# Performance work log

Hardware: AMD Instinct MI355X
Metric: run time of the kernel (lower is better)

The kernel has to match this reference:

```python
import jax, jax.numpy as jnp
import numpy as np


def gcn_conv(x, edge_index, W, b):
    # PyG GCNConv: h = x @ W; add self-loops; symmetric D^-1/2 (A+I) D^-1/2 aggregation; + bias
    n = x.shape[0]
    h = x @ W  # [N, out]
    loop = jnp.arange(n, dtype=edge_index.dtype)
    src = jnp.concatenate([edge_index[0], loop])  # message sources
    dst = jnp.concatenate([edge_index[1], loop])  # message targets
    ones = jnp.ones(dst.shape[0], dtype=h.dtype)
    deg = jax.ops.segment_sum(ones, dst, num_segments=n)  # in-degree incl. self-loop
    dinv = jnp.where(deg > 0, jax.lax.rsqrt(deg), 0.0)
    norm = dinv[src] * dinv[dst]  # [E+N]
    msg = h[src] * norm[:, None]  # gather + scale
    out = jax.ops.segment_sum(msg, dst, num_segments=n)  # scatter-add
    return out + b


def setup_inputs() -> dict:
    key = jax.random.key(0)
    ks = jax.random.split(key, 6)
    N, E, D = 100000, 600000, 128
    x = jax.random.normal(ks[0], (N, D), dtype=jnp.float32)
    edge_index = jax.random.randint(ks[1], (2, E), 0, N, dtype=jnp.int64)
    s = 1.0 / np.sqrt(D)
    W1 = jax.random.normal(ks[2], (D, D), dtype=jnp.float32) * s
    b1 = jnp.zeros((D,), dtype=jnp.float32)
    W2 = jax.random.normal(ks[3], (2 * D, D), dtype=jnp.float32) * (1.0 / np.sqrt(2 * D))
    b2 = jnp.zeros((D,), dtype=jnp.float32)
    Wout = jax.random.normal(ks[4], (D, 1), dtype=jnp.float32) * s
    bout = jnp.zeros((1,), dtype=jnp.float32)
    return {"x": x, "edge_index": edge_index, "W1": W1, "b1": b1,
            "W2": W2, "b2": b2, "Wout": Wout, "bout": bout}


def reference(x, edge_index, W1, b1, W2, b2, Wout, bout):
    y = gcn_conv(x, edge_index, W1, b1)          # [N, D]
    y = jnp.concatenate([x, y], axis=-1)          # [N, 2D]
    y = jax.nn.leaky_relu(y, negative_slope=0.01)
    z = gcn_conv(y, edge_index, W2, b2)           # [N, D]
    z = jax.nn.leaky_relu(z, negative_slope=0.01)
    return z @ Wout + bout                        # [N, 1]
```

## Files before the change

kernel.cpp:

```cpp
#include <hip/hip_runtime.h>

#define DIM 128
#define CAP 48

typedef _Float16 half8 __attribute__((ext_vector_type(8)));
typedef float f32x4 __attribute__((ext_vector_type(4)));

__device__ __forceinline__ float lrelu(float v) { return v > 0.f ? v : 0.01f * v; }

__device__ __forceinline__ void gather_sum(
    const _Float16* __restrict__ H, const int* __restrict__ sl,
    int cnt, int g, int zr, float a[8]) {
    int c16 = cnt < 16 ? cnt : 16;
    int sidb = (g < c16) ? sl[g] : zr;
    half8 v[8];
#pragma unroll
    for (int j = 0; j < 8; ++j) {
        int s = __shfl(sidb, j, 16);
        v[j] = *(const half8*)&H[(size_t)s * DIM + g * 8];
    }
#pragma unroll
    for (int j = 0; j < 8; ++j)
#pragma unroll
        for (int e = 0; e < 8; ++e) a[e] += (float)v[j][e];
    if (cnt > 8) {
#pragma unroll
        for (int j = 0; j < 8; ++j) {
            int s = __shfl(sidb, 8 + j, 16);
            v[j] = *(const half8*)&H[(size_t)s * DIM + g * 8];
        }
#pragma unroll
        for (int j = 0; j < 8; ++j)
#pragma unroll
            for (int e = 0; e < 8; ++e) a[e] += (float)v[j][e];
        if (cnt > 16) {
            for (int base = 16; base < cnt; base += 16) {
                int m = cnt - base;
                if (m > 16) m = 16;
                int sb = (g < m) ? sl[base + g] : zr;
                for (int j = 0; j < m; ++j) {
                    int s = __shfl(sb, j, 16);
                    half8 vv = *(const half8*)&H[(size_t)s * DIM + g * 8];
#pragma unroll
                    for (int e = 0; e < 8; ++e) a[e] += (float)vv[e];
                }
            }
        }
    }
}

__global__ __launch_bounds__(256) void k_prep(
    const int* __restrict__ src, const int* __restrict__ dst,
    int* __restrict__ cursor, int* __restrict__ srcs, int e, int eb,
    const float* __restrict__ W1, _Float16* __restrict__ Wp1,
    const float* __restrict__ W2, _Float16* __restrict__ Wp2,
    _Float16* __restrict__ zrow) {
    int b = blockIdx.x;
    if (b < eb) {
        int i = b * 256 + threadIdx.x;
        if (i < e) {
            int d = dst[i];
            int p = atomicAdd(&cursor[d], 1);
            if (p < CAP) srcs[(size_t)d * CAP + p] = src[i];
        }
        return;
    }
    b -= eb;
    if (b >= 192) {
        if (threadIdx.x < 16) {
            half8 z = 0;
            *(half8*)&zrow[threadIdx.x * 8] = z;
        }
        return;
    }
    const float* W;
    _Float16* Wp;
    int tid2;
    if (b < 64) { W = W1; Wp = Wp1; tid2 = b * 256 + threadIdx.x; }
    else        { W = W2; Wp = Wp2; tid2 = (b - 64) * 256 + threadIdx.x; }
    int jj = tid2 & 7;
    int frag = tid2 >> 3;
    int l = frag & 63;
    int cb = (frag >> 6) & 7;
    int kb = frag >> 9;
    int k = kb * 32 + ((l >> 4) << 3) + jj;
    int nn = cb * 16 + (l & 15);
    Wp[tid2] = (_Float16)W[(size_t)k * DIM + nn];
}

__global__ __launch_bounds__(256, 2) void k_mm1(
    const float* __restrict__ x, const _Float16* __restrict__ Wp1,
    const _Float16* __restrict__ Wp2, const int* __restrict__ cursor,
    _Float16* __restrict__ hs, _Float16* __restrict__ P, int n) {
    __shared__ _Float16 Hs[64 * 136];
    const int tid = threadIdx.x;
    const int w = tid >> 6, l = tid & 63;
    const int row0 = blockIdx.x * 64;
    const int arow = row0 + w * 16 + (l & 15);
    const int kq = (l >> 4) << 3;
    const bool ok = arow < n;
    const float* xr = &x[(size_t)arow * DIM + kq];

    f32x4 ah[8], ap[8];
#pragma unroll
    for (int cb = 0; cb < 8; ++cb) {
        f32x4 z = {0.f, 0.f, 0.f, 0.f};
        ah[cb] = z; ap[cb] = z;
    }

#pragma unroll
    for (int kb = 0; kb < 4; ++kb) {
        float4 v0 = make_float4(0.f, 0.f, 0.f, 0.f), v1 = v0;
        if (ok) {
            v0 = *(const float4*)&xr[kb * 32];
            v1 = *(const float4*)&xr[kb * 32 + 4];
        }
        half8 a, al;
        a[0] = (_Float16)v0.x; a[1] = (_Float16)v0.y;
        a[2] = (_Float16)v0.z; a[3] = (_Float16)v0.w;
        a[4] = (_Float16)v1.x; a[5] = (_Float16)v1.y;
        a[6] = (_Float16)v1.z; a[7] = (_Float16)v1.w;
#pragma unroll
        for (int e = 0; e < 8; ++e) {
            _Float16 t = a[e];
            al[e] = (t > (_Float16)0.f) ? t : t * (_Float16)0.01f;
        }
#pragma unroll
        for (int cb = 0; cb < 8; ++cb) {
            half8 bf = *(const half8*)&Wp1[((kb * 8 + cb) * 64 + l) * 8];
            ah[cb] = __builtin_amdgcn_mfma_f32_16x16x32_f16(a, bf, ah[cb], 0, 0, 0);
        }
#pragma unroll
        for (int cb = 0; cb < 8; ++cb) {
            half8 bf = *(const half8*)&Wp2[((kb * 8 + cb) * 64 + l) * 8];
            ap[cb] = __builtin_amdgcn_mfma_f32_16x16x32_f16(al, bf, ap[cb], 0, 0, 0);
        }
    }
    const int orow = w * 16 + ((l >> 4) << 2);
    const int oc = l & 15;
#pragma unroll
    for (int reg = 0; reg < 4; ++reg) {
        int grow = row0 + orow + reg;
        float d = (grow < n) ? rsqrtf((float)cursor[grow] + 1.0f) : 0.f;
#pragma unroll
        for (int cb = 0; cb < 8; ++cb)
            Hs[(orow + reg) * 136 + cb * 16 + oc] = (_Float16)(ah[cb][reg] * d);
    }
    __syncthreads();
#pragma unroll
    for (int it = 0; it < 4; ++it) {
        int i = it * 256 + tid;
        int r = i >> 4, c = (i & 15) * 8;
        if (row0 + r < n)
            *(half8*)&hs[(size_t)(row0 + r) * DIM + c] = *(const half8*)&Hs[r * 136 + c];
    }
    _Float16* pl = P + ((size_t)(blockIdx.x * 4 + w) * 64 + l) * 32;
#pragma unroll
    for (int c = 0; c < 4; ++c) {
        half8 o;
#pragma unroll
        for (int e = 0; e < 4; ++e) {
            o[e]     = (_Float16)ap[2 * c][e];
            o[4 + e] = (_Float16)ap[2 * c + 1][e];
        }
        *(half8*)&pl[c * 8] = o;
    }
}

__global__ __launch_bounds__(256, 2) void k_mm2g(
    const _Float16* __restrict__ hs, const int* __restrict__ cursor,
    const int* __restrict__ srcs, const float* __restrict__ b1,
    const _Float16* __restrict__ Wp2, const _Float16* __restrict__ P,
    _Float16* __restrict__ hs2, int n) {
    __shared__ _Float16 LS[64 * 136];
    const int tid = threadIdx.x;
    const int w = tid >> 6, l = tid & 63;
    const int g = tid & 15, gid = tid >> 4;
    const int row0 = blockIdx.x * 64;

    f32x4 acc[8];
    const _Float16* pl = P + ((size_t)(blockIdx.x * 4 + w) * 64 + l) * 32;
#pragma unroll
    for (int c = 0; c < 4; ++c) {
        half8 pv = *(const half8*)&pl[c * 8];
#pragma unroll
        for (int e = 0; e < 4; ++e) {
            acc[2 * c][e]     = (float)pv[e];
            acc[2 * c + 1][e] = (float)pv[4 + e];
        }
    }

#pragma unroll
    for (int it = 0; it < 4; ++it) {
        int node = row0 + it * 16 + gid;
        half8 o = 0;
        if (node < n) {
            int rawc = cursor[node];
            int cnt = rawc > CAP ? CAP : rawc;
            const int* sl = &srcs[(size_t)node * CAP];
            half8 h = *(const half8*)&hs[(size_t)node * DIM + g * 8];
            float a[8];
#pragma unroll
            for (int e = 0; e < 8; ++e) a[e] = (float)h[e];
            gather_sum(hs, sl, cnt, g, n, a);
            float d = rsqrtf((float)rawc + 1.0f);
            const float4 bb0 = *(const float4*)&b1[g * 8];
            const float4 bb1 = *(const float4*)&b1[g * 8 + 4];
            o[0] = (_Float16)lrelu(fmaf(a[0], d, bb0.x));
            o[1] = (_Float16)lrelu(fmaf(a[1], d, bb0.y));
            o[2] = (_Float16)lrelu(fmaf(a[2], d, bb0.z));
            o[3] = (_Float16)lrelu(fmaf(a[3], d, bb0.w));
            o[4] = (_Float16)lrelu(fmaf(a[4], d, bb1.x));
            o[5] = (_Float16)lrelu(fmaf(a[5], d, bb1.y));
            o[6] = (_Float16)lrelu(fmaf(a[6], d, bb1.z));
            o[7] = (_Float16)lrelu(fmaf(a[7], d, bb1.w));
        }
        *(half8*)&LS[(((it * 4 + (g >> 2)) * 64) + (g & 3) * 16 + gid) * 8] = o;
    }
    __syncthreads();

#pragma unroll
    for (int kb = 0; kb < 4; ++kb) {
        half8 a = *(const half8*)&LS[((w * 4 + kb) * 64 + l) * 8];
#pragma unroll
        for (int cb = 0; cb < 8; ++cb) {
            half8 bf = *(const half8*)&Wp2[(((kb + 4) * 8 + cb) * 64 + l) * 8];
            acc[cb] = __builtin_amdgcn_mfma_f32_16x16x32_f16(a, bf, acc[cb], 0, 0, 0);
        }
    }
    __syncthreads();
    const int orow = w * 16 + ((l >> 4) << 2);
    const int oc = l & 15;
#pragma unroll
    for (int reg = 0; reg < 4; ++reg) {
        int grow = row0 + orow + reg;
        float d = (grow < n) ? rsqrtf((float)cursor[grow] + 1.0f) : 0.f;
#pragma unroll
        for (int cb = 0; cb < 8; ++cb)
            LS[(orow + reg) * 136 + cb * 16 + oc] = (_Float16)(acc[cb][reg] * d);
    }
    __syncthreads();
#pragma unroll
    for (int it = 0; it < 4; ++it) {
        int i = it * 256 + tid;
        int r = i >> 4, c = (i & 15) * 8;
        if (row0 + r < n)
            *(half8*)&hs2[(size_t)(row0 + r) * DIM + c] = *(const half8*)&LS[r * 136 + c];
    }
}

__global__ __launch_bounds__(256) void k_gather2(
    const _Float16* __restrict__ hs2, const int* __restrict__ cursor,
    const int* __restrict__ srcs, const float* __restrict__ b2,
    const float* __restrict__ wout, const float* __restrict__ bout,
    float* __restrict__ out, int n) {
    const int node = blockIdx.x * 16 + (threadIdx.x >> 4);
    const int g = threadIdx.x & 15;
    if (node >= n) return;
    int rawc = cursor[node];
    int cnt = rawc > CAP ? CAP : rawc;
    const int* sl = &srcs[(size_t)node * CAP];
    half8 h = *(const half8*)&hs2[(size_t)node * DIM + g * 8];
    float a[8];
#pragma unroll
    for (int e = 0; e < 8; ++e) a[e] = (float)h[e];
    gather_sum(hs2, sl, cnt, g, n, a);
    float d = rsqrtf((float)rawc + 1.0f);
    const float4 bb0 = *(const float4*)&b2[g * 8];
    const float4 bb1 = *(const float4*)&b2[g * 8 + 4];
    const float4 wv0 = *(const float4*)&wout[g * 8];
    const float4 wv1 = *(const float4*)&wout[g * 8 + 4];
    float s = lrelu(fmaf(a[0], d, bb0.x)) * wv0.x + lrelu(fmaf(a[1], d, bb0.y)) * wv0.y +
              lrelu(fmaf(a[2], d, bb0.z)) * wv0.z + lrelu(fmaf(a[3], d, bb0.w)) * wv0.w +
              lrelu(fmaf(a[4], d, bb1.x)) * wv1.x + lrelu(fmaf(a[5], d, bb1.y)) * wv1.y +
              lrelu(fmaf(a[6], d, bb1.z)) * wv1.z + lrelu(fmaf(a[7], d, bb1.w)) * wv1.w;
#pragma unroll
    for (int off = 8; off > 0; off >>= 1) s += __shfl_down(s, off, 16);
    if (g == 0) out[node] = s + bout[0];
}

extern "C" void kernel_launch(void* const* d_in, const int* in_sizes, int n_in,
                              void* d_out, int out_size, void* d_ws, size_t ws_size,
                              hipStream_t stream) {
    const float* x    = (const float*)d_in[0];
    const int*   ei   = (const int*)d_in[1];
    const float* W1   = (const float*)d_in[2];
    const float* b1   = (const float*)d_in[3];
    const float* W2   = (const float*)d_in[4];
    const float* b2   = (const float*)d_in[5];
    const float* Wout = (const float*)d_in[6];
    const float* bout = (const float*)d_in[7];
    float* out = (float*)d_out;

    const int N = in_sizes[0] / DIM;
    const int E = in_sizes[1] / 2;
    const int* src = ei;
    const int* dst = ei + E;

    const int gb = (N + 63) / 64;
    const long long nx = (long long)N * DIM;

    size_t Na = ((size_t)N + 63) & ~(size_t)63;
    int* cursor   = (int*)d_ws;
    int* srcs     = cursor + Na;
    _Float16* Wp1 = (_Float16*)(srcs + (size_t)N * CAP);
    _Float16* Wp2 = Wp1 + 128 * 128;
    _Float16* hsb = Wp2 + 256 * 128;
    _Float16* Pb  = hsb + nx + DIM;

    const int eb = (E + 255) / 256;

    hipMemsetAsync(cursor, 0, (size_t)N * sizeof(int), stream);
    k_prep<<<eb + 193, 256, 0, stream>>>(src, dst, cursor, srcs, E, eb, W1, Wp1, W2, Wp2,
                                         hsb + nx);
    k_mm1<<<gb, 256, 0, stream>>>(x, Wp1, Wp2, cursor, hsb, Pb, N);
    k_mm2g<<<gb, 256, 0, stream>>>(hsb, cursor, srcs, b1, Wp2, Pb, Pb, N);
    k_gather2<<<(N + 15) / 16, 256, 0, stream>>>(Pb, cursor, srcs, b2, Wout, bout, out, N);
}
```

Before: 228.1 us.

## Fuse all stages into one persistent cooperative kernel with grid syncs

Replaces the memset plus four kernel launches with a single cooperative persistent kernel. It zeroes the cursors, packs the weights, builds the adjacency, runs both matmul/gather stages and the final gather, with grid-wide syncs between phases. The aim is to remove launch overhead and the tail gaps between kernels. In exchange, occupancy is capped by the cooperative grid size (launch_bounds 256,4). Grid syncs add latency, and blocks now loop over tiles, which may reduce latency hiding in the gather phases.

```diff
diff --git a/kernel.cpp b/kernel.cpp
--- a/kernel.cpp
+++ b/kernel.cpp
@@ -1,4 +1,7 @@
 #include <hip/hip_runtime.h>
+#include <hip/hip_cooperative_groups.h>
+
+namespace cg = cooperative_groups;
 
 #define DIM 128
 #define CAP 48
@@ -46,6 +49,245 @@
                 }
             }
         }
+    }
+}
+
+
+__device__ __forceinline__ void mm1_tile(
+    int tb, const float* __restrict__ x, const _Float16* __restrict__ Wp1,
+    const _Float16* __restrict__ Wp2, const int* __restrict__ cursor,
+    _Float16* __restrict__ hs, _Float16* __restrict__ P, int n, _Float16* Hs) {
+    const int tid = threadIdx.x;
+    const int w = tid >> 6, l = tid & 63;
+    const int row0 = tb * 64;
+    const int arow = row0 + w * 16 + (l & 15);
+    const int kq = (l >> 4) << 3;
+    const bool ok = arow < n;
+    const float* xr = &x[(size_t)arow * DIM + kq];
+
+    f32x4 ah[8], ap[8];
+#pragma unroll
+    for (int cb = 0; cb < 8; ++cb) {
+        f32x4 z = {0.f, 0.f, 0.f, 0.f};
+        ah[cb] = z; ap[cb] = z;
+    }
+
+#pragma unroll
+    for (int kb = 0; kb < 4; ++kb) {
+        float4 v0 = make_float4(0.f, 0.f, 0.f, 0.f), v1 = v0;
+        if (ok) {
+            v0 = *(const float4*)&xr[kb * 32];
+            v1 = *(const float4*)&xr[kb * 32 + 4];
+        }
+        half8 a, al;
+        a[0] = (_Float16)v0.x; a[1] = (_Float16)v0.y;
+        a[2] = (_Float16)v0.z; a[3] = (_Float16)v0.w;
+        a[4] = (_Float16)v1.x; a[5] = (_Float16)v1.y;
+        a[6] = (_Float16)v1.z; a[7] = (_Float16)v1.w;
+#pragma unroll
+        for (int e = 0; e < 8; ++e) {
+            _Float16 t = a[e];
+            al[e] = (t > (_Float16)0.f) ? t : t * (_Float16)0.01f;
+        }
+#pragma unroll
+        for (int cb = 0; cb < 8; ++cb) {
+            half8 bf = *(const half8*)&Wp1[((kb * 8 + cb) * 64 + l) * 8];
+            ah[cb] = __builtin_amdgcn_mfma_f32_16x16x32_f16(a, bf, ah[cb], 0, 0, 0);
+        }
+#pragma unroll
+        for (int cb = 0; cb < 8; ++cb) {
+            half8 bf = *(const half8*)&Wp2[((kb * 8 + cb) * 64 + l) * 8];
+            ap[cb] = __builtin_amdgcn_mfma_f32_16x16x32_f16(al, bf, ap[cb], 0, 0, 0);
+        }
+    }
+    const int orow = w * 16 + ((l >> 4) << 2);
+    const int oc = l & 15;
+#pragma unroll
+    for (int reg = 0; reg < 4; ++reg) {
+        int grow = row0 + orow + reg;
+        float d = (grow < n) ? rsqrtf((float)cursor[grow] + 1.0f) : 0.f;
+#pragma unroll
+        for (int cb = 0; cb < 8; ++cb)
+            Hs[(orow + reg) * 136 + cb * 16 + oc] = (_Float16)(ah[cb][reg] * d);
+    }
+    __syncthreads();
+#pragma unroll
+    for (int it = 0; it < 4; ++it) {
+        int i = it * 256 + tid;
+        int r = i >> 4, c = (i & 15) * 8;
+        if (row0 + r < n)
+            *(half8*)&hs[(size_t)(row0 + r) * DIM + c] = *(const half8*)&Hs[r * 136 + c];
+    }
+    _Float16* pl = P + ((size_t)(tb * 4 + w) * 64 + l) * 32;
+#pragma unroll
+    for (int c = 0; c < 4; ++c) {
+        half8 o;
+#pragma unroll
+        for (int e = 0; e < 4; ++e) {
+            o[e]     = (_Float16)ap[2 * c][e];
+            o[4 + e] = (_Float16)ap[2 * c + 1][e];
+        }
+        *(half8*)&pl[c * 8] = o;
+    }
+}
+
+__device__ __forceinline__ void mm2g_tile(
+    int tb, const _Float16* __restrict__ hs, const int* __restrict__ cursor,
+    const int* __restrict__ srcs, const float* __restrict__ b1,
+    const _Float16* __restrict__ Wp2, const _Float16* __restrict__ P,
+    _Float16* __restrict__ hs2, int n, _Float16* LS) {
+    const int tid = threadIdx.x;
+    const int w = tid >> 6, l = tid & 63;
+    const int g = tid & 15, gid = tid >> 4;
+    const int row0 = tb * 64;
+
+    f32x4 acc[8];
+    const _Float16* pl = P + ((size_t)(tb * 4 + w) * 64 + l) * 32;
+#pragma unroll
+    for (int c = 0; c < 4; ++c) {
+        half8 pv = *(const half8*)&pl[c * 8];
+#pragma unroll
+        for (int e = 0; e < 4; ++e) {
+            acc[2 * c][e]     = (float)pv[e];
+            acc[2 * c + 1][e] = (float)pv[4 + e];
+        }
+    }
+
+#pragma unroll
+    for (int it = 0; it < 4; ++it) {
+        int node = row0 + it * 16 + gid;
+        half8 o = 0;
+        if (node < n) {
+            int rawc = cursor[node];
+            int cnt = rawc > CAP ? CAP : rawc;
+            const int* sl = &srcs[(size_t)node * CAP];
+            half8 h = *(const half8*)&hs[(size_t)node * DIM + g * 8];
+            float a[8];
+#pragma unroll
+            for (int e = 0; e < 8; ++e) a[e] = (float)h[e];
+            gather_sum(hs, sl, cnt, g, n, a);
+            float d = rsqrtf((float)rawc + 1.0f);
+            const float4 bb0 = *(const float4*)&b1[g * 8];
+            const float4 bb1 = *(const float4*)&b1[g * 8 + 4];
+            o[0] = (_Float16)lrelu(fmaf(a[0], d, bb0.x));
+            o[1] = (_Float16)lrelu(fmaf(a[1], d, bb0.y));
+            o[2] = (_Float16)lrelu(fmaf(a[2], d, bb0.z));
+            o[3] = (_Float16)lrelu(fmaf(a[3], d, bb0.w));
+            o[4] = (_Float16)lrelu(fmaf(a[4], d, bb1.x));
+            o[5] = (_Float16)lrelu(fmaf(a[5], d, bb1.y));
+            o[6] = (_Float16)lrelu(fmaf(a[6], d, bb1.z));
+            o[7] = (_Float16)lrelu(fmaf(a[7], d, bb1.w));
+        }
+        *(half8*)&LS[(((it * 4 + (g >> 2)) * 64) + (g & 3) * 16 + gid) * 8] = o;
+    }
+    __syncthreads();
+
+#pragma unroll
+    for (int kb = 0; kb < 4; ++kb) {
+        half8 a = *(const half8*)&LS[((w * 4 + kb) * 64 + l) * 8];
+#pragma unroll
+        for (int cb = 0; cb < 8; ++cb) {
+            half8 bf = *(const half8*)&Wp2[(((kb + 4) * 8 + cb) * 64 + l) * 8];
+            acc[cb] = __builtin_amdgcn_mfma_f32_16x16x32_f16(a, bf, acc[cb], 0, 0, 0);
+        }
+    }
+    __syncthreads();
+    const int orow = w * 16 + ((l >> 4) << 2);
+    const int oc = l & 15;
+#pragma unroll
+    for (int reg = 0; reg < 4; ++reg) {
+        int grow = row0 + orow + reg;
+        float d = (grow < n) ? rsqrtf((float)cursor[grow] + 1.0f) : 0.f;
+#pragma unroll
+        for (int cb = 0; cb < 8; ++cb)
+            LS[(orow + reg) * 136 + cb * 16 + oc] = (_Float16)(acc[cb][reg] * d);
+    }
+    __syncthreads();
+#pragma unroll
+    for (int it = 0; it < 4; ++it) {
+        int i = it * 256 + tid;
+        int r = i >> 4, c = (i & 15) * 8;
+        if (row0 + r < n)
+            *(half8*)&hs2[(size_t)(row0 + r) * DIM + c] = *(const half8*)&LS[r * 136 + c];
+    }
+}
+
+__device__ __forceinline__ void gather2_grp(
+    int base, const _Float16* __restrict__ hs2, const int* __restrict__ cursor,
+    const int* __restrict__ srcs, const float* __restrict__ b2,
+    const float* __restrict__ wout, const float* __restrict__ bout,
+    float* __restrict__ out, int n) {
+    const int node = base + (threadIdx.x >> 4);
+    const int g = threadIdx.x & 15;
+    if (node >= n) return;
+    int rawc = cursor[node];
+    int cnt = rawc > CAP ? CAP : rawc;
+    const int* sl = &srcs[(size_t)node * CAP];
+    half8 h = *(const half8*)&hs2[(size_t)node * DIM + g * 8];
+    float a[8];
+#pragma unroll
+    for (int e = 0; e < 8; ++e) a[e] = (float)h[e];
+    gather_sum(hs2, sl, cnt, g, n, a);
+    float d = rsqrtf((float)rawc + 1.0f);
+    const float4 bb0 = *(const float4*)&b2[g * 8];
+    const float4 bb1 = *(const float4*)&b2[g * 8 + 4];
+    const float4 wv0 = *(const float4*)&wout[g * 8];
+    const float4 wv1 = *(const float4*)&wout[g * 8 + 4];
+    float s = lrelu(fmaf(a[0], d, bb0.x)) * wv0.x + lrelu(fmaf(a[1], d, bb0.y)) * wv0.y +
+              lrelu(fmaf(a[2], d, bb0.z)) * wv0.z + lrelu(fmaf(a[3], d, bb0.w)) * wv0.w +
+              lrelu(fmaf(a[4], d, bb1.x)) * wv1.x + lrelu(fmaf(a[5], d, bb1.y)) * wv1.y +
+              lrelu(fmaf(a[6], d, bb1.z)) * wv1.z + lrelu(fmaf(a[7], d, bb1.w)) * wv1.w;
+#pragma unroll
+    for (int off = 8; off > 0; off >>= 1) s += __shfl_down(s, off, 16);
+    if (g == 0) out[node] = s + bout[0];
+}
+
+__global__ __launch_bounds__(256, 4) void k_fused(
+    const float* __restrict__ x, const int* __restrict__ esrc, const int* __restrict__ edst,
+    int E, const float* __restrict__ W1, const float* __restrict__ b1,
+    const float* __restrict__ W2, const float* __restrict__ b2,
+    const float* __restrict__ Wout, const float* __restrict__ bout,
+    float* __restrict__ out, int* __restrict__ cursor, int* __restrict__ srcs,
+    _Float16* __restrict__ Wp1, _Float16* __restrict__ Wp2,
+    _Float16* __restrict__ hs, _Float16* __restrict__ P, int n, int gb) {
+    __shared__ _Float16 LS[64 * 136];
+    const int tid = threadIdx.x;
+    const int nb = gridDim.x;
+    const int gtid = blockIdx.x * 256 + tid;
+    const int gstride = nb * 256;
+
+    for (int i = gtid; i < n; i += gstride) cursor[i] = 0;
+    if (blockIdx.x == 0 && tid < 16) {
+        half8 z = 0;
+        *(half8*)&hs[(size_t)n * DIM + tid * 8] = z;
+    }
+    for (int t = gtid; t < 49152; t += gstride) {
+        const float* W; _Float16* Wp; int t2;
+        if (t < 16384) { W = W1; Wp = Wp1; t2 = t; }
+        else           { W = W2; Wp = Wp2; t2 = t - 16384; }
+        int jj = t2 & 7, frag = t2 >> 3;
+        int l = frag & 63, cb = (frag >> 6) & 7, kb = frag >> 9;
+        Wp[t2] = (_Float16)W[(size_t)(kb * 32 + ((l >> 4) << 3) + jj) * DIM + cb * 16 + (l & 15)];
+    }
+    cg::this_grid().sync();
+    for (int i = gtid; i < E; i += gstride) {
+        int d = edst[i];
+        int p = atomicAdd(&cursor[d], 1);
+        if (p < CAP) srcs[(size_t)d * CAP + p] = esrc[i];
+    }
+    cg::this_grid().sync();
+    for (int tb = blockIdx.x; tb < gb; tb += nb) {
+        mm1_tile(tb, x, Wp1, Wp2, cursor, hs, P, n, LS);
+        __syncthreads();
+    }
+    cg::this_grid().sync();
+    for (int tb = blockIdx.x; tb < gb; tb += nb) {
+        mm2g_tile(tb, hs, cursor, srcs, b1, Wp2, P, P, n, LS);
+        __syncthreads();
+    }
+    cg::this_grid().sync();
+    for (int base = blockIdx.x * 16; base < n; base += nb * 16) {
+        gather2_grp(base, P, cursor, srcs, b2, Wout, bout, out, n);
     }
 }
 
@@ -83,9 +325,7 @@
     int l = frag & 63;
     int cb = (frag >> 6) & 7;
     int kb = frag >> 9;
-    int k = kb * 32 + ((l >> 4) << 3) + jj;
-    int nn = cb * 16 + (l & 15);
-    Wp[tid2] = (_Float16)W[(size_t)k * DIM + nn];
+    Wp[tid2] = (_Float16)W[(size_t)(kb * 32 + ((l >> 4) << 3) + jj) * DIM + cb * 16 + (l & 15)];
 }
 
 __global__ __launch_bounds__(256, 2) void k_mm1(
@@ -93,78 +333,7 @@
     const _Float16* __restrict__ Wp2, const int* __restrict__ cursor,
     _Float16* __restrict__ hs, _Float16* __restrict__ P, int n) {
     __shared__ _Float16 Hs[64 * 136];
-    const int tid = threadIdx.x;
-    const int w = tid >> 6, l = tid & 63;
-    const int row0 = blockIdx.x * 64;
-    const int arow = row0 + w * 16 + (l & 15);
-    const int kq = (l >> 4) << 3;
-    const bool ok = arow < n;
-    const float* xr = &x[(size_t)arow * DIM + kq];
-
-    f32x4 ah[8], ap[8];
-#pragma unroll
-    for (int cb = 0; cb < 8; ++cb) {
-        f32x4 z = {0.f, 0.f, 0.f, 0.f};
-        ah[cb] = z; ap[cb] = z;
-    }
-
-#pragma unroll
-    for (int kb = 0; kb < 4; ++kb) {
-        float4 v0 = make_float4(0.f, 0.f, 0.f, 0.f), v1 = v0;
-        if (ok) {
-            v0 = *(const float4*)&xr[kb * 32];
-            v1 = *(const float4*)&xr[kb * 32 + 4];
-        }
-        half8 a, al;
-        a[0] = (_Float16)v0.x; a[1] = (_Float16)v0.y;
-        a[2] = (_Float16)v0.z; a[3] = (_Float16)v0.w;
-        a[4] = (_Float16)v1.x; a[5] = (_Float16)v1.y;
-        a[6] = (_Float16)v1.z; a[7] = (_Float16)v1.w;
-#pragma unroll
-        for (int e = 0; e < 8; ++e) {
-            _Float16 t = a[e];
-            al[e] = (t > (_Float16)0.f) ? t : t * (_Float16)0.01f;
-        }
-#pragma unroll
-        for (int cb = 0; cb < 8; ++cb) {
-            half8 bf = *(const half8*)&Wp1[((kb * 8 + cb) * 64 + l) * 8];
-            ah[cb] = __builtin_amdgcn_mfma_f32_16x16x32_f16(a, bf, ah[cb], 0, 0, 0);
-        }
-#pragma unroll
-        for (int cb = 0; cb < 8; ++cb) {
-            half8 bf = *(const half8*)&Wp2[((kb * 8 + cb) * 64 + l) * 8];
-            ap[cb] = __builtin_amdgcn_mfma_f32_16x16x32_f16(al, bf, ap[cb], 0, 0, 0);
-        }
-    }
-    const int orow = w * 16 + ((l >> 4) << 2);
-    const int oc = l & 15;
-#pragma unroll
-    for (int reg = 0; reg < 4; ++reg) {
-        int grow = row0 + orow + reg;
-        float d = (grow < n) ? rsqrtf((float)cursor[grow] + 1.0f) : 0.f;
-#pragma unroll
-        for (int cb = 0; cb < 8; ++cb)
-            Hs[(orow + reg) * 136 + cb * 16 + oc] = (_Float16)(ah[cb][reg] * d);
-    }
-    __syncthreads();
-#pragma unroll
-    for (int it = 0; it < 4; ++it) {
-        int i = it * 256 + tid;
-        int r = i >> 4, c = (i & 15) * 8;
-        if (row0 + r < n)
-            *(half8*)&hs[(size_t)(row0 + r) * DIM + c] = *(const half8*)&Hs[r * 136 + c];
-    }
-    _Float16* pl = P + ((size_t)(blockIdx.x * 4 + w) * 64 + l) * 32;
-#pragma unroll
-    for (int c = 0; c < 4; ++c) {
-        half8 o;
-#pragma unroll
-        for (int e = 0; e < 4; ++e) {
-            o[e]     = (_Float16)ap[2 * c][e];
-            o[4 + e] = (_Float16)ap[2 * c + 1][e];
-        }
-        *(half8*)&pl[c * 8] = o;
-    }
+    mm1_tile(blockIdx.x, x, Wp1, Wp2, cursor, hs, P, n, Hs);
 }
 
 __global__ __launch_bounds__(256, 2) void k_mm2g(
@@ -173,80 +342,7 @@
     const _Float16* __restrict__ Wp2, const _Float16* __restrict__ P,
     _Float16* __restrict__ hs2, int n) {
     __shared__ _Float16 LS[64 * 136];
-    const int tid = threadIdx.x;
-    const int w = tid >> 6, l = tid & 63;
-    const int g = tid & 15, gid = tid >> 4;
-    const int row0 = blockIdx.x * 64;
-
-    f32x4 acc[8];
-    const _Float16* pl = P + ((size_t)(blockIdx.x * 4 + w) * 64 + l) * 32;
-#pragma unroll
-    for (int c = 0; c < 4; ++c) {
-        half8 pv = *(const half8*)&pl[c * 8];
-#pragma unroll
-        for (int e = 0; e < 4; ++e) {
-            acc[2 * c][e]     = (float)pv[e];
-            acc[2 * c + 1][e] = (float)pv[4 + e];
-        }
-    }
-
-#pragma unroll
-    for (int it = 0; it < 4; ++it) {
-        int node = row0 + it * 16 + gid;
-        half8 o = 0;
-        if (node < n) {
-            int rawc = cursor[node];
-            int cnt = rawc > CAP ? CAP : rawc;
-            const int* sl = &srcs[(size_t)node * CAP];
-            half8 h = *(const half8*)&hs[(size_t)node * DIM + g * 8];
-            float a[8];
-#pragma unroll
-            for (int e = 0; e < 8; ++e) a[e] = (float)h[e];
-            gather_sum(hs, sl, cnt, g, n, a);
-            float d = rsqrtf((float)rawc + 1.0f);
-            const float4 bb0 = *(const float4*)&b1[g * 8];
-            const float4 bb1 = *(const float4*)&b1[g * 8 + 4];
-            o[0] = (_Float16)lrelu(fmaf(a[0], d, bb0.x));
-            o[1] = (_Float16)lrelu(fmaf(a[1], d, bb0.y));
-            o[2] = (_Float16)lrelu(fmaf(a[2], d, bb0.z));
-            o[3] = (_Float16)lrelu(fmaf(a[3], d, bb0.w));
-            o[4] = (_Float16)lrelu(fmaf(a[4], d, bb1.x));
-            o[5] = (_Float16)lrelu(fmaf(a[5], d, bb1.y));
-            o[6] = (_Float16)lrelu(fmaf(a[6], d, bb1.z));
-            o[7] = (_Float16)lrelu(fmaf(a[7], d, bb1.w));
-        }
-        *(half8*)&LS[(((it * 4 + (g >> 2)) * 64) + (g & 3) * 16 + gid) * 8] = o;
-    }
-    __syncthreads();
-
-#pragma unroll
-    for (int kb = 0; kb < 4; ++kb) {
-        half8 a = *(const half8*)&LS[((w * 4 + kb) * 64 + l) * 8];
-#pragma unroll
-        for (int cb = 0; cb < 8; ++cb) {
-            half8 bf = *(const half8*)&Wp2[(((kb + 4) * 8 + cb) * 64 + l) * 8];
-            acc[cb] = __builtin_amdgcn_mfma_f32_16x16x32_f16(a, bf, acc[cb], 0, 0, 0);
-        }
-    }
-    __syncthreads();
-    const int orow = w * 16 + ((l >> 4) << 2);
-    const int oc = l & 15;
-#pragma unroll
-    for (int reg = 0; reg < 4; ++reg) {
-        int grow = row0 + orow + reg;
-        float d = (grow < n) ? rsqrtf((float)cursor[grow] + 1.0f) : 0.f;
-#pragma unroll
-        for (int cb = 0; cb < 8; ++cb)
-            LS[(orow + reg) * 136 + cb * 16 + oc] = (_Float16)(acc[cb][reg] * d);
-    }
-    __syncthreads();
-#pragma unroll
-    for (int it = 0; it < 4; ++it) {
-        int i = it * 256 + tid;
-        int r = i >> 4, c = (i & 15) * 8;
-        if (row0 + r < n)
-            *(half8*)&hs2[(size_t)(row0 + r) * DIM + c] = *(const half8*)&LS[r * 136 + c];
-    }
+    mm2g_tile(blockIdx.x, hs, cursor, srcs, b1, Wp2, P, hs2, n, LS);
 }
 
 __global__ __launch_bounds__(256) void k_gather2(
@@ -254,29 +350,7 @@
     const int* __restrict__ srcs, const float* __restrict__ b2,
     const float* __restrict__ wout, const float* __restrict__ bout,
     float* __restrict__ out, int n) {
-    const int node = blockIdx.x * 16 + (threadIdx.x >> 4);
-    const int g = threadIdx.x & 15;
-    if (node >= n) return;
-    int rawc = cursor[node];
-    int cnt = rawc > CAP ? CAP : rawc;
-    const int* sl = &srcs[(size_t)node * CAP];
-    half8 h = *(const half8*)&hs2[(size_t)node * DIM + g * 8];
-    float a[8];
-#pragma unroll
-    for (int e = 0; e < 8; ++e) a[e] = (float)h[e];
-    gather_sum(hs2, sl, cnt, g, n, a);
-    float d = rsqrtf((float)rawc + 1.0f);
-    const float4 bb0 = *(const float4*)&b2[g * 8];
-    const float4 bb1 = *(const float4*)&b2[g * 8 + 4];
-    const float4 wv0 = *(const float4*)&wout[g * 8];
-    const float4 wv1 = *(const float4*)&wout[g * 8 + 4];
-    float s = lrelu(fmaf(a[0], d, bb0.x)) * wv0.x + lrelu(fmaf(a[1], d, bb0.y)) * wv0.y +
-              lrelu(fmaf(a[2], d, bb0.z)) * wv0.z + lrelu(fmaf(a[3], d, bb0.w)) * wv0.w +
-              lrelu(fmaf(a[4], d, bb1.x)) * wv1.x + lrelu(fmaf(a[5], d, bb1.y)) * wv1.y +
-              lrelu(fmaf(a[6], d, bb1.z)) * wv1.z + lrelu(fmaf(a[7], d, bb1.w)) * wv1.w;
-#pragma unroll
-    for (int off = 8; off > 0; off >>= 1) s += __shfl_down(s, off, 16);
-    if (g == 0) out[node] = s + bout[0];
+    gather2_grp(blockIdx.x * 16, hs2, cursor, srcs, b2, wout, bout, out, n);
 }
 
 extern "C" void kernel_launch(void* const* d_in, const int* in_sizes, int n_in,
@@ -308,12 +382,41 @@
     _Float16* hsb = Wp2 + 256 * 128;
     _Float16* Pb  = hsb + nx + DIM;
 
-    const int eb = (E + 255) / 256;
-
-    hipMemsetAsync(cursor, 0, (size_t)N * sizeof(int), stream);
-    k_prep<<<eb + 193, 256, 0, stream>>>(src, dst, cursor, srcs, E, eb, W1, Wp1, W2, Wp2,
-                                         hsb + nx);
-    k_mm1<<<gb, 256, 0, stream>>>(x, Wp1, Wp2, cursor, hsb, Pb, N);
-    k_mm2g<<<gb, 256, 0, stream>>>(hsb, cursor, srcs, b1, Wp2, Pb, Pb, N);
-    k_gather2<<<(N + 15) / 16, 256, 0, stream>>>(Pb, cursor, srcs, b2, Wout, bout, out, N);
-}
+    static int coop_blocks = -2;
+    if (coop_blocks == -2) {
+        int nbpc = 0;
+        if (hipOccupancyMaxActiveBlocksPerMultiprocessor(
+                &nbpc, reinterpret_cast<const void*>(k_fused), 256, 0) != hipSuccess || nbpc < 1)
+            nbpc = 0;
+        if (nbpc > 8) nbpc = 8;
+        int ncu = 256;
+        hipDeviceProp_t prop;
+        if (hipGetDeviceProperties(&prop, 0) == hipSuccess && prop.multiProcessorCount > 0)
+            ncu = prop.multiProcessorCount;
+        coop_blocks = nbpc > 0 ? nbpc * ncu : -1;
+    }
+
+    bool launched = false;
+    if (coop_blocks > 0) {
+        int E_ = E, N_ = N, gb_ = gb;
+        void* args[] = {(void*)&x, (void*)&src, (void*)&dst, (void*)&E_,
+                        (void*)&W1, (void*)&b1, (void*)&W2, (void*)&b2,
+                        (void*)&Wout, (void*)&bout, (void*)&out,
+                        (void*)&cursor, (void*)&srcs, (void*)&Wp1, (void*)&Wp2,
+                        (void*)&hsb, (void*)&Pb, (void*)&N_, (void*)&gb_};
+        if (hipLaunchCooperativeKernel(reinterpret_cast<const void*>(k_fused),
+                                       dim3(coop_blocks), dim3(256), args, 0, stream) == hipSuccess)
+            launched = true;
+        else
+            coop_blocks = -1;
+    }
+    if (!launched) {
+        const int eb = (E + 255) / 256;
+        hipMemsetAsync(cursor, 0, (size_t)N * sizeof(int), stream);
+        k_prep<<<eb + 193, 256, 0, stream>>>(src, dst, cursor, srcs, E, eb, W1, Wp1, W2, Wp2,
+                                             hsb + nx);
+        k_mm1<<<gb, 256, 0, stream>>>(x, Wp1, Wp2, cursor, hsb, Pb, N);
+        k_mm2g<<<gb, 256, 0, stream>>>(hsb, cursor, srcs, b1, Wp2, Pb, Pb, N);
+        k_gather2<<<(N + 15) / 16, 256, 0, stream>>>(Pb, cursor, srcs, b2, Wout, bout, out, N);
+    }
+}
```

Measured after the change: 646.1 us. 183% more time.

## Overlap edge bucketing with first matmul and move source normalization into gather

Applied to the files above, without the earlier changes.

Edge bucketing (the atomic cursor increments and srcs writes) moves out of the prep kernel and into extra blocks of the first matmul kernel, so CSR building runs alongside the GEMM. Because degrees are not final during that GEMM, the per-row D^-1/2 scaling of h is dropped there and applied per source inside the layer-1 gather, using a shuffled rsqrt of each neighbor's cursor. The hipMemset is replaced by zeroing inside the init kernel, which removes one stream operation. The cost is an extra cursor load and rsqrt per gathered group, plus an FMA instead of an add per element.

```diff
diff --git a/kernel.cpp b/kernel.cpp
--- a/kernel.cpp
+++ b/kernel.cpp
@@ -49,23 +49,66 @@
     }
 }
 
-__global__ __launch_bounds__(256) void k_prep(
-    const int* __restrict__ src, const int* __restrict__ dst,
-    int* __restrict__ cursor, int* __restrict__ srcs, int e, int eb,
+__device__ __forceinline__ void gather_sum_scaled(
+    const _Float16* __restrict__ H, const int* __restrict__ cursor,
+    const int* __restrict__ sl, int cnt, int g, int zr, float a[8]) {
+    int c16 = cnt < 16 ? cnt : 16;
+    int sidb = (g < c16) ? sl[g] : zr;
+    float dvb = rsqrtf((float)cursor[sidb] + 1.0f);
+    half8 v[8];
+#pragma unroll
+    for (int j = 0; j < 8; ++j) {
+        int s = __shfl(sidb, j, 16);
+        v[j] = *(const half8*)&H[(size_t)s * DIM + g * 8];
+    }
+#pragma unroll
+    for (int j = 0; j < 8; ++j) {
+        float sc = __shfl(dvb, j, 16);
+#pragma unroll
+        for (int e = 0; e < 8; ++e) a[e] = fmaf((float)v[j][e], sc, a[e]);
+    }
+    if (cnt > 8) {
+#pragma unroll
+        for (int j = 0; j < 8; ++j) {
+            int s = __shfl(sidb, 8 + j, 16);
+            v[j] = *(const half8*)&H[(size_t)s * DIM + g * 8];
+        }
+#pragma unroll
+        for (int j = 0; j < 8; ++j) {
+            float sc = __shfl(dvb, 8 + j, 16);
+#pragma unroll
+            for (int e = 0; e < 8; ++e) a[e] = fmaf((float)v[j][e], sc, a[e]);
+        }
+        if (cnt > 16) {
+            for (int base = 16; base < cnt; base += 16) {
+                int m = cnt - base;
+                if (m > 16) m = 16;
+                int sb = (g < m) ? sl[base + g] : zr;
+                float db2 = rsqrtf((float)cursor[sb] + 1.0f);
+                for (int j = 0; j < m; ++j) {
+                    int s = __shfl(sb, j, 16);
+                    float sc = __shfl(db2, j, 16);
+                    half8 vv = *(const half8*)&H[(size_t)s * DIM + g * 8];
+#pragma unroll
+                    for (int e = 0; e < 8; ++e) a[e] = fmaf((float)vv[e], sc, a[e]);
+                }
+            }
+        }
+    }
+}
+
+__global__ __launch_bounds__(256) void k_init(
+    int* __restrict__ cursor, int na, int nzb,
     const float* __restrict__ W1, _Float16* __restrict__ Wp1,
     const float* __restrict__ W2, _Float16* __restrict__ Wp2,
     _Float16* __restrict__ zrow) {
     int b = blockIdx.x;
-    if (b < eb) {
+    if (b < nzb) {
         int i = b * 256 + threadIdx.x;
-        if (i < e) {
-            int d = dst[i];
-            int p = atomicAdd(&cursor[d], 1);
-            if (p < CAP) srcs[(size_t)d * CAP + p] = src[i];
-        }
+        if (i < na) cursor[i] = 0;
         return;
     }
-    b -= eb;
+    b -= nzb;
     if (b >= 192) {
         if (threadIdx.x < 16) {
             half8 z = 0;
@@ -83,19 +126,29 @@
     int l = frag & 63;
     int cb = (frag >> 6) & 7;
     int kb = frag >> 9;
-    int k = kb * 32 + ((l >> 4) << 3) + jj;
-    int nn = cb * 16 + (l & 15);
-    Wp[tid2] = (_Float16)W[(size_t)k * DIM + nn];
-}
-
-__global__ __launch_bounds__(256, 2) void k_mm1(
+    Wp[tid2] = (_Float16)W[(size_t)(kb * 32 + ((l >> 4) << 3) + jj) * DIM + cb * 16 + (l & 15)];
+}
+
+__global__ __launch_bounds__(256, 2) void k_front(
     const float* __restrict__ x, const _Float16* __restrict__ Wp1,
-    const _Float16* __restrict__ Wp2, const int* __restrict__ cursor,
-    _Float16* __restrict__ hs, _Float16* __restrict__ P, int n) {
+    const _Float16* __restrict__ Wp2, _Float16* __restrict__ hs,
+    _Float16* __restrict__ P, int n, int gb,
+    const int* __restrict__ esrc, const int* __restrict__ edst,
+    int* __restrict__ cursor, int* __restrict__ srcs, int E) {
     __shared__ _Float16 Hs[64 * 136];
+    const int bb = blockIdx.x;
+    if (bb >= gb) {
+        int i = (bb - gb) * 256 + threadIdx.x;
+        if (i < E) {
+            int d = edst[i];
+            int p = atomicAdd(&cursor[d], 1);
+            if (p < CAP) srcs[(size_t)d * CAP + p] = esrc[i];
+        }
+        return;
+    }
     const int tid = threadIdx.x;
     const int w = tid >> 6, l = tid & 63;
-    const int row0 = blockIdx.x * 64;
+    const int row0 = bb * 64;
     const int arow = row0 + w * 16 + (l & 15);
     const int kq = (l >> 4) << 3;
     const bool ok = arow < n;
@@ -140,11 +193,9 @@
     const int oc = l & 15;
 #pragma unroll
     for (int reg = 0; reg < 4; ++reg) {
-        int grow = row0 + orow + reg;
-        float d = (grow < n) ? rsqrtf((float)cursor[grow] + 1.0f) : 0.f;
 #pragma unroll
         for (int cb = 0; cb < 8; ++cb)
-            Hs[(orow + reg) * 136 + cb * 16 + oc] = (_Float16)(ah[cb][reg] * d);
+            Hs[(orow + reg) * 136 + cb * 16 + oc] = (_Float16)ah[cb][reg];
     }
     __syncthreads();
 #pragma unroll
@@ -154,7 +205,7 @@
         if (row0 + r < n)
             *(half8*)&hs[(size_t)(row0 + r) * DIM + c] = *(const half8*)&Hs[r * 136 + c];
     }
-    _Float16* pl = P + ((size_t)(blockIdx.x * 4 + w) * 64 + l) * 32;
+    _Float16* pl = P + ((size_t)(bb * 4 + w) * 64 + l) * 32;
 #pragma unroll
     for (int c = 0; c < 4; ++c) {
         half8 o;
@@ -198,12 +249,12 @@
             int rawc = cursor[node];
             int cnt = rawc > CAP ? CAP : rawc;
             const int* sl = &srcs[(size_t)node * CAP];
+            float d = rsqrtf((float)rawc + 1.0f);
             half8 h = *(const half8*)&hs[(size_t)node * DIM + g * 8];
             float a[8];
 #pragma unroll
-            for (int e = 0; e < 8; ++e) a[e] = (float)h[e];
-            gather_sum(hs, sl, cnt, g, n, a);
-            float d = rsqrtf((float)rawc + 1.0f);
+            for (int e = 0; e < 8; ++e) a[e] = (float)h[e] * d;
+            gather_sum_scaled(hs, cursor, sl, cnt, g, n, a);
             const float4 bb0 = *(const float4*)&b1[g * 8];
             const float4 bb1 = *(const float4*)&b1[g * 8 + 4];
             o[0] = (_Float16)lrelu(fmaf(a[0], d, bb0.x));
@@ -309,11 +360,10 @@
     _Float16* Pb  = hsb + nx + DIM;
 
     const int eb = (E + 255) / 256;
-
-    hipMemsetAsync(cursor, 0, (size_t)N * sizeof(int), stream);
-    k_prep<<<eb + 193, 256, 0, stream>>>(src, dst, cursor, srcs, E, eb, W1, Wp1, W2, Wp2,
-                                         hsb + nx);
-    k_mm1<<<gb, 256, 0, stream>>>(x, Wp1, Wp2, cursor, hsb, Pb, N);
+    const int nzb = ((int)Na + 255) / 256;
+
+    k_init<<<nzb + 193, 256, 0, stream>>>(cursor, (int)Na, nzb, W1, Wp1, W2, Wp2, hsb + nx);
+    k_front<<<gb + eb, 256, 0, stream>>>(x, Wp1, Wp2, hsb, Pb, N, gb, src, dst, cursor, srcs, E);
     k_mm2g<<<gb, 256, 0, stream>>>(hsb, cursor, srcs, b1, Wp2, Pb, Pb, N);
     k_gather2<<<(N + 15) / 16, 256, 0, stream>>>(Pb, cursor, srcs, b2, Wout, bout, out, N);
 }
```

After: 217.7 us. 4.6% less time.
